# Performance work log

Hardware: AMD Instinct MI355X
Metric: run time of the kernel (lower is better)

## Reference

```python
import jax, jax.numpy as jnp
import numpy as np

EPS_ATTN = 1e-6
EPS_LN = 1e-5


def _layer_norm(x, g, b):
    m = jnp.mean(x, axis=-1, keepdims=True)
    v = jnp.mean((x - m) ** 2, axis=-1, keepdims=True)
    return (x - m) * jax.lax.rsqrt(v + EPS_LN) * g + b


def _linear_attention(q, k, v):
    # q,k,v: [N, L/S, H, D]; elu feature map (+1 keeps values positive)
    q = jax.nn.elu(q) + 1.0
    k = jax.nn.elu(k) + 1.0
    s_len = v.shape[1]
    v = v / s_len
    kv = jnp.einsum('nshd,nshv->nhdv', k, v)            # [N,H,D,D]
    z = 1.0 / (jnp.einsum('nlhd,nhd->nlh', q, k.sum(axis=1)) + EPS_ATTN)
    out = jnp.einsum('nlhd,nhdv->nlhv', q, kv) * z[..., None] * s_len
    return out


def setup_inputs() -> dict:
    key = jax.random.key(0)
    ks = jax.random.split(key, 8)
    N, L, S, H, D = 4, 4096, 4096, 8, 64
    sc = 0.05
    return {
        'x': jax.random.normal(ks[0], (N, L, H, D), jnp.float32),
        'source': jax.random.normal(ks[1], (N, S, H, D), jnp.float32),
        'wq': jax.random.normal(ks[2], (D, D), jnp.float32) * sc,
        'wk': jax.random.normal(ks[3], (D, D), jnp.float32) * sc,
        'wv': jax.random.normal(ks[4], (D, D), jnp.float32) * sc,
        'wmerge': jax.random.normal(ks[5], (D, D), jnp.float32) * sc,
        'w1': jax.random.normal(ks[6], (2 * D, 2 * D), jnp.float32) * sc,
        'w2': jax.random.normal(ks[7], (D, 2 * D), jnp.float32) * sc,
        'g1': jnp.ones((D,), jnp.float32),
        'b1': jnp.zeros((D,), jnp.float32),
        'g2': jnp.ones((D,), jnp.float32),
        'b2': jnp.zeros((D,), jnp.float32),
    }


def reference(x, source, wq, wk, wv, wmerge, w1, w2, g1, b1, g2, b2):
    # projections (torch Linear: y = x @ W.T), applied on last dim D=d_model
    q = jnp.einsum('nlhd,ed->nlhe', x, wq)
    k = jnp.einsum('nshd,ed->nshe', source, wk)
    v = jnp.einsum('nshd,ed->nshe', source, wv)
    message = _linear_attention(q, k, v)                # [N,L,H,D]
    message = jnp.einsum('nlhd,ed->nlhe', message, wmerge)
    message = _layer_norm(message, g1, b1)
    h = jnp.concatenate([x, message], axis=-1)          # [N,L,H,2D]
    h = jax.nn.relu(jnp.einsum('nlhd,ed->nlhe', h, w1))
    h = jnp.einsum('nlhd,ed->nlhe', h, w2)              # [N,L,H,D]
    h = _layer_norm(h, g2, b2)
    return x + h
```

## Files before the change

kernel.cpp:

```cpp
#include <hip/hip_runtime.h>
#include <cstdint>

#define NB 4
#define LL 4096
#define SS 4096
#define HH 8
#define DD 64
#define NHC (NB*HH)
#define KVCH 16

typedef unsigned short ushort_t;
typedef __bf16 bf16x8 __attribute__((ext_vector_type(8)));
typedef float f32x4 __attribute__((ext_vector_type(4)));
typedef unsigned short u16x8 __attribute__((ext_vector_type(8)));
typedef unsigned short u16x4 __attribute__((ext_vector_type(4)));

__device__ __forceinline__ float bf2f(unsigned short u) {
    union { unsigned int i; float f; } v; v.i = ((unsigned int)u) << 16; return v.f;
}
__device__ __forceinline__ unsigned short f2bf(float f) {
    union { __bf16 b; unsigned short u; } v; v.b = (__bf16)f; return v.u;
}
__device__ __forceinline__ bool input_is_bf16(const void* g1) {
    return ((const unsigned short*)g1)[0] == 0x3F80u;
}

template<bool BF16>
__device__ __forceinline__ float ldgf(const void* p, size_t i) {
    if constexpr (BF16) return bf2f(((const unsigned short*)p)[i]);
    else                return ((const float*)p)[i];
}
template<bool BF16>
__device__ __forceinline__ u16x8 ld8(const void* p, size_t i) {
    if constexpr (BF16) {
        return *reinterpret_cast<const u16x8*>((const unsigned short*)p + i);
    } else {
        const f32x4* f4 = reinterpret_cast<const f32x4*>((const float*)p + i);
        f32x4 a = f4[0], b = f4[1];
        u16x8 o;
        #pragma unroll
        for (int j = 0; j < 4; ++j) { o[j] = f2bf(a[j]); o[4 + j] = f2bf(b[j]); }
        return o;
    }
}
__device__ __forceinline__ bf16x8 ldsA(const ushort_t* p) {
    return *reinterpret_cast<const bf16x8*>(p);
}
#define MFMA16(a,b,c) __builtin_amdgcn_mfma_f32_16x16x32_bf16(a,b,c,0,0,0)

template<bool BF16, int LC>
__device__ __forceinline__ void stage_w(const void* g, size_t goff, ushort_t* dst,
                                        int rows, int dstride, int tid) {
    int total8 = (rows << LC) >> 3;
    for (int i8 = tid; i8 < total8; i8 += 256) {
        int i = i8 << 3;
        int r = i >> LC, c = i & ((1 << LC) - 1);
        *reinterpret_cast<u16x8*>(dst + r * dstride + c) = ld8<BF16>(g, goff + i);
    }
}

__device__ __forceinline__ void red16(float v[4]) {
    #pragma unroll
    for (int m = 1; m < 16; m <<= 1) {
        #pragma unroll
        for (int r = 0; r < 4; ++r) v[r] += __shfl_xor(v[r], m);
    }
}

template<bool BF16, bool PART>
__device__ void kv_body(const void* __restrict__ src, const void* __restrict__ wk,
                        const void* __restrict__ wv, float* __restrict__ kvg,
                        float* __restrict__ ksumg,
                        ushort_t* S, ushort_t* KT, ushort_t* VT, float* KS)
{
    const int tid = threadIdx.x;
    const int lane = tid & 63, w = tid >> 6;
    const int lg = lane >> 4, l15 = lane & 15;
    const int bid = blockIdx.x;
    const int nh = bid >> 4, ch = bid & 15;
    const int n = nh >> 3, h = nh & 7;
    const int s0 = ch * 256;
    const f32x4 z4 = {0.f, 0.f, 0.f, 0.f};

    stage_w<BF16, 6>(wk, 0, KT, 64, 136, tid);
    stage_w<BF16, 6>(wv, 0, VT, 64, 136, tid);
    for (int i8 = tid; i8 < 1024; i8 += 256) {
        int r = i8 >> 3, c8 = (i8 & 7) << 3;
        size_t gb = ((size_t)((size_t)n * SS + (s0 + r)) * HH + h) * DD + c8;
        *reinterpret_cast<u16x8*>(S + r * 72 + c8) = ld8<BF16>(src, gb);
    }
    __syncthreads();

    bf16x8 wkf[2][4], wvf[2][4];
    #pragma unroll
    for (int ks = 0; ks < 2; ++ks)
        #pragma unroll
        for (int nt = 0; nt < 4; ++nt) {
            wkf[ks][nt] = ldsA(KT + (nt * 16 + l15) * 136 + ks * 32 + lg * 8);
            wvf[ks][nt] = ldsA(VT + (nt * 16 + l15) * 136 + ks * 32 + lg * 8);
        }
    __syncthreads();

    f32x4 kvacc[4];
    #pragma unroll
    for (int nt = 0; nt < 4; ++nt) kvacc[nt] = z4;
    float ksp[4] = {0.f, 0.f, 0.f, 0.f};

    for (int st = 0; st < 2; ++st) {
        #pragma unroll
        for (int mtt = 0; mtt < 2; ++mtt) {
            const int rowA = w * 32 + mtt * 16;
            bf16x8 af[2];
            #pragma unroll
            for (int ks = 0; ks < 2; ++ks)
                af[ks] = ldsA(S + (rowA + l15) * 72 + ks * 32 + lg * 8);
            f32x4 ka[4], va[4];
            #pragma unroll
            for (int nt = 0; nt < 4; ++nt) { ka[nt] = z4; va[nt] = z4; }
            __builtin_amdgcn_s_setprio(1);
            #pragma unroll
            for (int ks = 0; ks < 2; ++ks)
                #pragma unroll
                for (int nt = 0; nt < 4; ++nt) {
                    ka[nt] = MFMA16(af[ks], wkf[ks][nt], ka[nt]);
                    va[nt] = MFMA16(af[ks], wvf[ks][nt], va[nt]);
                }
            __builtin_amdgcn_s_setprio(0);
            #pragma unroll
            for (int nt = 0; nt < 4; ++nt) {
                u16x4 kp, vp;
                #pragma unroll
                for (int r = 0; r < 4; ++r) {
                    float kvl = ka[nt][r];
                    kvl = kvl > 0.f ? kvl + 1.f : __expf(kvl);
                    ksp[nt] += kvl;
                    kp[r] = f2bf(kvl);
                    vp[r] = f2bf(va[nt][r]);
                }
                const int dcol = nt * 16 + l15;
                *reinterpret_cast<u16x4*>(KT + dcol * 136 + rowA + lg * 4) = kp;
                *reinterpret_cast<u16x4*>(VT + dcol * 136 + rowA + lg * 4) = vp;
            }
        }
        __syncthreads();

        if (st == 0) {
            for (int i8 = tid; i8 < 1024; i8 += 256) {
                int r = i8 >> 3, c8 = (i8 & 7) << 3;
                size_t gb = ((size_t)((size_t)n * SS + (s0 + 128 + r)) * HH + h) * DD + c8;
                *reinterpret_cast<u16x8*>(S + r * 72 + c8) = ld8<BF16>(src, gb);
            }
        }
        __builtin_amdgcn_s_setprio(1);
        #pragma unroll
        for (int ks = 0; ks < 4; ++ks) {
            bf16x8 akv = ldsA(KT + (w * 16 + l15) * 136 + ks * 32 + lg * 8);
            #pragma unroll
            for (int nt = 0; nt < 4; ++nt) {
                bf16x8 bkv = ldsA(VT + (nt * 16 + l15) * 136 + ks * 32 + lg * 8);
                kvacc[nt] = MFMA16(akv, bkv, kvacc[nt]);
            }
        }
        __builtin_amdgcn_s_setprio(0);
        __syncthreads();
    }

    if constexpr (PART) {
        float* kvo = kvg + (size_t)bid * 4096;
        #pragma unroll
        for (int nt = 0; nt < 4; ++nt)
            #pragma unroll
            for (int r = 0; r < 4; ++r)
                kvo[(w * 16 + lg * 4 + r) * DD + nt * 16 + l15] = kvacc[nt][r];
    } else {
        float* kvo = kvg + (size_t)nh * 4096;
        #pragma unroll
        for (int nt = 0; nt < 4; ++nt)
            #pragma unroll
            for (int r = 0; r < 4; ++r)
                atomicAdd(&kvo[(w * 16 + lg * 4 + r) * DD + nt * 16 + l15], kvacc[nt][r]);
    }
    #pragma unroll
    for (int m = 16; m < 64; m <<= 1)
        #pragma unroll
        for (int nt = 0; nt < 4; ++nt) ksp[nt] += __shfl_xor(ksp[nt], m);
    if (lane < 16) {
        #pragma unroll
        for (int nt = 0; nt < 4; ++nt) KS[w * 64 + nt * 16 + lane] = ksp[nt];
    }
    __syncthreads();
    if (tid < 64) {
        float s = KS[tid] + KS[64 + tid] + KS[128 + tid] + KS[192 + tid];
        if constexpr (PART) ksumg[(size_t)bid * 64 + tid] = s;
        else                atomicAdd(&ksumg[nh * 64 + tid], s);
    }
}

template<bool PART>
__global__ __launch_bounds__(256, 2) void kv_kernel(
    const void* __restrict__ src, const void* __restrict__ wk, const void* __restrict__ wv,
    const void* __restrict__ g1, float* __restrict__ kvg, float* __restrict__ ksumg)
{
    __shared__ ushort_t S[128 * 72];
    __shared__ ushort_t KT[64 * 136];
    __shared__ ushort_t VT[64 * 136];
    __shared__ float    KS[4 * 64];
    if (input_is_bf16(g1)) kv_body<true , PART>(src, wk, wv, kvg, ksumg, S, KT, VT, KS);
    else                   kv_body<false, PART>(src, wk, wv, kvg, ksumg, S, KT, VT, KS);
}

template<bool BF16, bool PART>
__device__ void main_body(const void* __restrict__ x,
                          const void* __restrict__ wq, const void* __restrict__ wm,
                          const void* __restrict__ w1, const void* __restrict__ w2,
                          const void* __restrict__ g1, const void* __restrict__ b1,
                          const void* __restrict__ g2, const void* __restrict__ b2,
                          const float* __restrict__ kvg, const float* __restrict__ ksumg,
                          void* __restrict__ outp,
                          ushort_t* w1s, ushort_t* kvs, ushort_t* B0, ushort_t* B1,
                          ushort_t* B2)
{
    const int tid = threadIdx.x;
    const int lane = tid & 63, w = tid >> 6;
    const int lg = lane >> 4, l15 = lane & 15;
    const int bid = blockIdx.x;
    const int nh = bid >> 4, ch = bid & 15;
    const int n = nh >> 3, h = nh & 7;
    const int rowA = w * 16;
    const f32x4 z4 = {0.f, 0.f, 0.f, 0.f};

    auto ldx = [&](int t, u16x8 xv[2]) {
        #pragma unroll
        for (int p = 0; p < 2; ++p) {
            int r16 = p * 8 + (lane >> 3), c8 = (lane & 7) << 3;
            size_t gb = ((size_t)((size_t)n * LL + (ch * 256 + t * 64 + rowA + r16)) * HH + h) * DD + c8;
            xv[p] = ld8<BF16>(x, gb);
        }
    };

    u16x8 xv[2];
    ldx(0, xv);

    stage_w<BF16, 6>(wq, 0, B0, 64, 72, tid);
    stage_w<BF16, 6>(wm, 0, B1, 64, 72, tid);
    stage_w<BF16, 7>(w2, 0, w1s, 64, 136, tid);
    if constexpr (PART) {
        for (int i4 = tid; i4 < 1024; i4 += 256) {
            const float* base = kvg + (size_t)nh * KVCH * 4096 + i4 * 4;
            f32x4 s = z4;
            #pragma unroll
            for (int c = 0; c < KVCH; ++c)
                s += *reinterpret_cast<const f32x4*>(base + c * 4096);
            int d = i4 >> 4, e4 = (i4 * 4) & 63;
            u16x4 pk;
            #pragma unroll
            for (int j = 0; j < 4; ++j) pk[j] = f2bf(s[j]);
            *reinterpret_cast<u16x4*>(B2 + d * 72 + e4) = pk;
        }
    } else {
        for (int i = tid; i < 4096; i += 256) {
            int d = i >> 6, e = i & 63;
            B2[d * 72 + e] = f2bf(kvg[(size_t)nh * 4096 + i]);
        }
    }
    __syncthreads();

    bf16x8 wqf[2][4], w2f[4][4];
    #pragma unroll
    for (int ks = 0; ks < 2; ++ks)
        #pragma unroll
        for (int nt = 0; nt < 4; ++nt)
            wqf[ks][nt] = ldsA(B0 + (nt * 16 + l15) * 72 + ks * 32 + lg * 8);
    #pragma unroll
    for (int ks = 0; ks < 4; ++ks)
        #pragma unroll
        for (int nt = 0; nt < 4; ++nt)
            w2f[ks][nt] = ldsA(w1s + (nt * 16 + l15) * 136 + ks * 32 + lg * 8);
    {
        bf16x8 akv[2];
        #pragma unroll
        for (int ks = 0; ks < 2; ++ks)
            akv[ks] = ldsA(B2 + (w * 16 + l15) * 72 + ks * 32 + lg * 8);
        f32x4 km[4];
        #pragma unroll
        for (int nt = 0; nt < 4; ++nt) km[nt] = z4;
        #pragma unroll
        for (int ks = 0; ks < 2; ++ks)
            #pragma unroll
            for (int nt = 0; nt < 4; ++nt) {
                bf16x8 bwm = ldsA(B1 + (nt * 16 + l15) * 72 + ks * 32 + lg * 8);
                km[nt] = MFMA16(akv[ks], bwm, km[nt]);
            }
        #pragma unroll
        for (int nt = 0; nt < 4; ++nt)
            #pragma unroll
            for (int r = 0; r < 4; ++r)
                kvs[(nt * 16 + l15) * 72 + w * 16 + lg * 4 + r] = f2bf(km[nt][r]);
    }
    __syncthreads();

    stage_w<BF16, 7>(w1, 0, w1s, 128, 136, tid);
    bf16x8 kvmf[2][4];
    #pragma unroll
    for (int ks = 0; ks < 2; ++ks)
        #pragma unroll
        for (int nt = 0; nt < 4; ++nt)
            kvmf[ks][nt] = ldsA(kvs + (nt * 16 + l15) * 72 + ks * 32 + lg * 8);
    float g1r[4], b1r[4], g2r[4], b2r[4], ksr[4];
    #pragma unroll
    for (int nt = 0; nt < 4; ++nt) {
        int c = nt * 16 + l15;
        g1r[nt] = ldgf<BF16>(g1, c); b1r[nt] = ldgf<BF16>(b1, c);
        g2r[nt] = ldgf<BF16>(g2, c); b2r[nt] = ldgf<BF16>(b2, c);
        if constexpr (PART) {
            float s = 0.f;
            #pragma unroll
            for (int cc = 0; cc < KVCH; ++cc)
                s += ksumg[((size_t)nh * KVCH + cc) * 64 + c];
            ksr[nt] = s;
        } else {
            ksr[nt] = ksumg[nh * 64 + c];
        }
    }
    __syncthreads();

    for (int t = 0; t < 4; ++t) {
        const int l0 = ch * 256 + t * 64;

        #pragma unroll
        for (int p = 0; p < 2; ++p) {
            int r16 = p * 8 + (lane >> 3), c8 = (lane & 7) << 3;
            *reinterpret_cast<u16x8*>(B0 + (rowA + r16) * 72 + c8) = xv[p];
        }
        u16x8 xn[2];
        if (t < 3) ldx(t + 1, xn);

        bf16x8 af[2];
        #pragma unroll
        for (int ks = 0; ks < 2; ++ks)
            af[ks] = ldsA(B0 + (rowA + l15) * 72 + ks * 32 + lg * 8);
        f32x4 qa[4];
        #pragma unroll
        for (int nt = 0; nt < 4; ++nt) qa[nt] = z4;
        __builtin_amdgcn_s_setprio(1);
        #pragma unroll
        for (int ks = 0; ks < 2; ++ks)
            #pragma unroll
            for (int nt = 0; nt < 4; ++nt)
                qa[nt] = MFMA16(af[ks], wqf[ks][nt], qa[nt]);
        __builtin_amdgcn_s_setprio(0);
        float zp[4] = {0.f, 0.f, 0.f, 0.f};
        #pragma unroll
        for (int nt = 0; nt < 4; ++nt)
            #pragma unroll
            for (int r = 0; r < 4; ++r) {
                float v = qa[nt][r];
                v = v > 0.f ? v + 1.f : __expf(v);
                zp[r] += v * ksr[nt];
                B1[(rowA + lg * 4 + r) * 72 + nt * 16 + l15] = f2bf(v);
            }
        red16(zp);
        float zr[4];
        #pragma unroll
        for (int r = 0; r < 4; ++r) zr[r] = 1.f / (zp[r] + 1e-6f);

        #pragma unroll
        for (int ks = 0; ks < 2; ++ks)
            af[ks] = ldsA(B1 + (rowA + l15) * 72 + ks * 32 + lg * 8);
        f32x4 ma[4];
        #pragma unroll
        for (int nt = 0; nt < 4; ++nt) ma[nt] = z4;
        __builtin_amdgcn_s_setprio(1);
        #pragma unroll
        for (int ks = 0; ks < 2; ++ks)
            #pragma unroll
            for (int nt = 0; nt < 4; ++nt)
                ma[nt] = MFMA16(af[ks], kvmf[ks][nt], ma[nt]);
        __builtin_amdgcn_s_setprio(0);
        #pragma unroll
        for (int nt = 0; nt < 4; ++nt)
            #pragma unroll
            for (int r = 0; r < 4; ++r) ma[nt][r] *= zr[r];

        float s1[4] = {0.f,0.f,0.f,0.f}, s2[4] = {0.f,0.f,0.f,0.f};
        #pragma unroll
        for (int nt = 0; nt < 4; ++nt)
            #pragma unroll
            for (int r = 0; r < 4; ++r) {
                float v = ma[nt][r]; s1[r] += v; s2[r] += v * v;
            }
        red16(s1); red16(s2);
        #pragma unroll
        for (int r = 0; r < 4; ++r) {
            float mu = s1[r] * 0.015625f;
            float var = s2[r] * 0.015625f - mu * mu;
            s1[r] = mu; s2[r] = rsqrtf(var + 1e-5f);
        }
        #pragma unroll
        for (int nt = 0; nt < 4; ++nt)
            #pragma unroll
            for (int r = 0; r < 4; ++r)
                B1[(rowA + lg * 4 + r) * 72 + nt * 16 + l15] =
                    f2bf((ma[nt][r] - s1[r]) * s2[r] * g1r[nt] + b1r[nt]);

        f32x4 ha[4];
        #pragma unroll
        for (int nt = 0; nt < 4; ++nt) ha[nt] = z4;
        #pragma unroll
        for (int half = 0; half < 2; ++half) {
            f32x4 ta[4];
            #pragma unroll
            for (int nt = 0; nt < 4; ++nt) ta[nt] = z4;
            __builtin_amdgcn_s_setprio(1);
            #pragma unroll
            for (int ks = 0; ks < 4; ++ks) {
                const ushort_t* bp = (ks < 2) ? B0 : B1;
                bf16x8 a1 = ldsA(bp + (rowA + l15) * 72 + (ks & 1) * 32 + lg * 8);
                #pragma unroll
                for (int nt = 0; nt < 4; ++nt) {
                    bf16x8 bw = ldsA(w1s + (half * 64 + nt * 16 + l15) * 136 + ks * 32 + lg * 8);
                    ta[nt] = MFMA16(a1, bw, ta[nt]);
                }
            }
            __builtin_amdgcn_s_setprio(0);
            #pragma unroll
            for (int nt = 0; nt < 4; ++nt)
                #pragma unroll
                for (int r = 0; r < 4; ++r)
                    B2[(rowA + lg * 4 + r) * 72 + nt * 16 + l15] =
                        f2bf(fmaxf(ta[nt][r], 0.f));
            __builtin_amdgcn_s_setprio(1);
            #pragma unroll
            for (int k2 = 0; k2 < 2; ++k2) {
                bf16x8 a2 = ldsA(B2 + (rowA + l15) * 72 + k2 * 32 + lg * 8);
                #pragma unroll
                for (int nt = 0; nt < 4; ++nt)
                    ha[nt] = MFMA16(a2, w2f[half * 2 + k2][nt], ha[nt]);
            }
            __builtin_amdgcn_s_setprio(0);
        }

        float t1[4] = {0.f,0.f,0.f,0.f}, t2[4] = {0.f,0.f,0.f,0.f};
        #pragma unroll
        for (int nt = 0; nt < 4; ++nt)
            #pragma unroll
            for (int r = 0; r < 4; ++r) {
                float v = ha[nt][r]; t1[r] += v; t2[r] += v * v;
            }
        red16(t1); red16(t2);
        #pragma unroll
        for (int r = 0; r < 4; ++r) {
            float mu = t1[r] * 0.015625f;
            float var = t2[r] * 0.015625f - mu * mu;
            t1[r] = mu; t2[r] = rsqrtf(var + 1e-5f);
        }
        #pragma unroll
        for (int nt = 0; nt < 4; ++nt)
            #pragma unroll
            for (int r = 0; r < 4; ++r) {
                float xv2 = bf2f(B0[(rowA + lg * 4 + r) * 72 + nt * 16 + l15]);
                float ov = xv2 + (ha[nt][r] - t1[r]) * t2[r] * g2r[nt] + b2r[nt];
                B1[(rowA + lg * 4 + r) * 72 + nt * 16 + l15] = f2bf(ov);
            }

        #pragma unroll
        for (int p = 0; p < 2; ++p) {
            int r16 = p * 8 + (lane >> 3), c8 = (lane & 7) << 3;
            size_t gb = ((size_t)((size_t)n * LL + (l0 + rowA + r16)) * HH + h) * DD + c8;
            u16x8 v = *reinterpret_cast<const u16x8*>(B1 + (rowA + r16) * 72 + c8);
            if constexpr (BF16) {
                *reinterpret_cast<u16x8*>((unsigned short*)outp + gb) = v;
            } else {
                float* fo = (float*)outp + gb;
                f32x4 lo, hi;
                #pragma unroll
                for (int j = 0; j < 4; ++j) { lo[j] = bf2f(v[j]); hi[j] = bf2f(v[4 + j]); }
                *reinterpret_cast<f32x4*>(fo) = lo;
                *reinterpret_cast<f32x4*>(fo + 4) = hi;
            }
        }

        if (t < 3) { xv[0] = xn[0]; xv[1] = xn[1]; }
    }
}

template<bool PART>
__global__ __launch_bounds__(256, 2) void main_kernel(
    const void* __restrict__ x,
    const void* __restrict__ wq, const void* __restrict__ wm,
    const void* __restrict__ w1, const void* __restrict__ w2,
    const void* __restrict__ g1, const void* __restrict__ b1,
    const void* __restrict__ g2, const void* __restrict__ b2,
    const float* __restrict__ kvg, const float* __restrict__ ksumg,
    void* __restrict__ outp)
{
    __shared__ ushort_t w1s[128 * 136];
    __shared__ ushort_t kvs[64 * 72];
    __shared__ ushort_t B0[64 * 72];
    __shared__ ushort_t B1[64 * 72];
    __shared__ ushort_t B2[64 * 72];
    if (input_is_bf16(g1))
        main_body<true , PART>(x, wq, wm, w1, w2, g1, b1, g2, b2, kvg, ksumg, outp,
                               w1s, kvs, B0, B1, B2);
    else
        main_body<false, PART>(x, wq, wm, w1, w2, g1, b1, g2, b2, kvg, ksumg, outp,
                               w1s, kvs, B0, B1, B2);
}

extern "C" void kernel_launch(void* const* d_in, const int* in_sizes, int n_in,
                              void* d_out, int out_size, void* d_ws, size_t ws_size,
                              hipStream_t stream) {
    const void* x   = d_in[0];
    const void* src = d_in[1];
    const void* wq  = d_in[2];
    const void* wk  = d_in[3];
    const void* wv  = d_in[4];
    const void* wm  = d_in[5];
    const void* w1  = d_in[6];
    const void* w2  = d_in[7];
    const void* g1  = d_in[8];
    const void* b1  = d_in[9];
    const void* g2  = d_in[10];
    const void* b2  = d_in[11];

    const size_t kv_elems   = (size_t)NHC * KVCH * 4096;
    const size_t ksum_elems = (size_t)NHC * KVCH * 64;
    const size_t need = (kv_elems + ksum_elems) * sizeof(float);

    if (ws_size >= need) {
        float* kvp = (float*)d_ws;
        float* ksp = kvp + kv_elems;
        kv_kernel<true ><<<NHC * KVCH, 256, 0, stream>>>(src, wk, wv, g1, kvp, ksp);
        main_kernel<true ><<<NHC * 16, 256, 0, stream>>>(x, wq, wm, w1, w2, g1, b1,
                                                         g2, b2, kvp, ksp, d_out);
    } else {
        float* kvg   = (float*)d_ws;
        float* ksumg = kvg + (size_t)NHC * DD * DD;
        hipMemsetAsync(d_ws, 0, ((size_t)NHC * DD * DD + NHC * DD) * sizeof(float), stream);
        kv_kernel<false><<<NHC * KVCH, 256, 0, stream>>>(src, wk, wv, g1, kvg, ksumg);
        main_kernel<false><<<NHC * 16, 256, 0, stream>>>(x, wq, wm, w1, w2, g1, b1,
                                                         g2, b2, kvg, ksumg, d_out);
    }
}
```

Measured before the change: 160.5 us.

## Split KV reduction into separate kernel, double main grid, swizzle LDS

Adds a reduce kernel that sums the per-chunk KV partials, multiplies by wmerge once per head and writes a bf16 transposed result plus ksum to workspace. Previously every main-kernel block redid this reduction and small GEMM. The main kernel now runs with twice as many blocks, each handling 128 rows, and uses XOR-swizzled unpadded LDS layouts. It also splits the FFN hidden dimension into four 32-wide pieces to shrink the B2 buffer, with launch bounds raised to 3 blocks per CU for higher occupancy. The cost is an extra kernel launch and a workspace round trip for the reduced KV.

```diff
diff --git a/kernel.cpp b/kernel.cpp
--- a/kernel.cpp
+++ b/kernel.cpp
@@ -48,6 +48,9 @@
 }
 #define MFMA16(a,b,c) __builtin_amdgcn_mfma_f32_16x16x32_bf16(a,b,c,0,0,0)
 
+__device__ __forceinline__ int sw64(int r, int c)  { return (r << 6) + (c ^ ((r & 7) << 3)); }
+__device__ __forceinline__ int sw128(int r, int c) { return (r << 7) + (c ^ ((r & 7) << 3)); }
+
 template<bool BF16, int LC>
 __device__ __forceinline__ void stage_w(const void* g, size_t goff, ushort_t* dst,
                                         int rows, int dstride, int tid) {
@@ -56,6 +59,17 @@
         int i = i8 << 3;
         int r = i >> LC, c = i & ((1 << LC) - 1);
         *reinterpret_cast<u16x8*>(dst + r * dstride + c) = ld8<BF16>(g, goff + i);
+    }
+}
+template<bool BF16, int LC>
+__device__ __forceinline__ void stage_sw(const void* g, ushort_t* dst, int rows, int tid) {
+    int total8 = (rows << LC) >> 3;
+    for (int i8 = tid; i8 < total8; i8 += 256) {
+        int i = i8 << 3;
+        int r = i >> LC, c = i & ((1 << LC) - 1);
+        int off;
+        if constexpr (LC == 6) off = sw64(r, c); else off = sw128(r, c);
+        *reinterpret_cast<u16x8*>(dst + off) = ld8<BF16>(g, i);
     }
 }
 
@@ -209,22 +223,91 @@
     else                   kv_body<false, PART>(src, wk, wv, kvg, ksumg, S, KT, VT, KS);
 }
 
-template<bool BF16, bool PART>
+template<bool BF16, int NCH>
+__device__ void reduce_body(const float* __restrict__ kvp, const float* __restrict__ ksp,
+                            const void* __restrict__ wm,
+                            ushort_t* __restrict__ kvmT, float* __restrict__ ksumf,
+                            ushort_t* KVS, ushort_t* WMS)
+{
+    const int tid = threadIdx.x;
+    const int lane = tid & 63, w = tid >> 6;
+    const int lg = lane >> 4, l15 = lane & 15;
+    const int nh = blockIdx.x;
+    const f32x4 z4 = {0.f, 0.f, 0.f, 0.f};
+
+    stage_w<BF16, 6>(wm, 0, WMS, 64, 72, tid);
+    for (int i4 = tid; i4 < 1024; i4 += 256) {
+        const float* base = kvp + (size_t)nh * NCH * 4096 + i4 * 4;
+        f32x4 s = z4;
+        #pragma unroll
+        for (int c = 0; c < NCH; ++c)
+            s += *reinterpret_cast<const f32x4*>(base + c * 4096);
+        int d = i4 >> 4, e4 = (i4 & 15) * 4;
+        u16x4 pk;
+        #pragma unroll
+        for (int j = 0; j < 4; ++j) pk[j] = f2bf(s[j]);
+        *reinterpret_cast<u16x4*>(KVS + d * 72 + e4) = pk;
+    }
+    if (tid < 64) {
+        float s = 0.f;
+        #pragma unroll
+        for (int c = 0; c < NCH; ++c) s += ksp[((size_t)nh * NCH + c) * 64 + tid];
+        ksumf[nh * 64 + tid] = s;
+    }
+    __syncthreads();
+
+    bf16x8 akv[2];
+    #pragma unroll
+    for (int ks = 0; ks < 2; ++ks)
+        akv[ks] = ldsA(KVS + (w * 16 + l15) * 72 + ks * 32 + lg * 8);
+    f32x4 km[4];
+    #pragma unroll
+    for (int nt = 0; nt < 4; ++nt) km[nt] = z4;
+    #pragma unroll
+    for (int ks = 0; ks < 2; ++ks)
+        #pragma unroll
+        for (int nt = 0; nt < 4; ++nt) {
+            bf16x8 bwm = ldsA(WMS + (nt * 16 + l15) * 72 + ks * 32 + lg * 8);
+            km[nt] = MFMA16(akv[ks], bwm, km[nt]);
+        }
+    #pragma unroll
+    for (int nt = 0; nt < 4; ++nt) {
+        u16x4 pk;
+        #pragma unroll
+        for (int r = 0; r < 4; ++r) pk[r] = f2bf(km[nt][r]);
+        *reinterpret_cast<u16x4*>(kvmT + (size_t)nh * 4096 + (nt * 16 + l15) * 64
+                                  + w * 16 + lg * 4) = pk;
+    }
+}
+
+template<int NCH>
+__global__ __launch_bounds__(256, 4) void reduce_kernel(
+    const float* __restrict__ kvp, const float* __restrict__ ksp,
+    const void* __restrict__ wm, const void* __restrict__ g1,
+    ushort_t* __restrict__ kvmT, float* __restrict__ ksumf)
+{
+    __shared__ ushort_t KVS[64 * 72];
+    __shared__ ushort_t WMS[64 * 72];
+    if (input_is_bf16(g1)) reduce_body<true , NCH>(kvp, ksp, wm, kvmT, ksumf, KVS, WMS);
+    else                   reduce_body<false, NCH>(kvp, ksp, wm, kvmT, ksumf, KVS, WMS);
+}
+
+template<bool BF16>
 __device__ void main_body(const void* __restrict__ x,
-                          const void* __restrict__ wq, const void* __restrict__ wm,
+                          const void* __restrict__ wq,
                           const void* __restrict__ w1, const void* __restrict__ w2,
                           const void* __restrict__ g1, const void* __restrict__ b1,
                           const void* __restrict__ g2, const void* __restrict__ b2,
-                          const float* __restrict__ kvg, const float* __restrict__ ksumg,
+                          const ushort_t* __restrict__ kvmT,
+                          const float* __restrict__ ksumf,
                           void* __restrict__ outp,
-                          ushort_t* w1s, ushort_t* kvs, ushort_t* B0, ushort_t* B1,
-                          ushort_t* B2)
+                          ushort_t* w1s, ushort_t* B0, ushort_t* B1, ushort_t* B2)
 {
     const int tid = threadIdx.x;
     const int lane = tid & 63, w = tid >> 6;
     const int lg = lane >> 4, l15 = lane & 15;
     const int bid = blockIdx.x;
-    const int nh = bid >> 4, ch = bid & 15;
+    const int nh = bid >> 5, ch = bid & 31;
     const int n = nh >> 3, h = nh & 7;
     const int rowA = w * 16;
     const f32x4 z4 = {0.f, 0.f, 0.f, 0.f};
@@ -233,7 +316,7 @@
         #pragma unroll
         for (int p = 0; p < 2; ++p) {
             int r16 = p * 8 + (lane >> 3), c8 = (lane & 7) << 3;
-            size_t gb = ((size_t)((size_t)n * LL + (ch * 256 + t * 64 + rowA + r16)) * HH + h) * DD + c8;
+            size_t gb = ((size_t)((size_t)n * LL + (ch * 128 + t * 64 + rowA + r16)) * HH + h) * DD + c8;
             xv[p] = ld8<BF16>(x, gb);
         }
     };
@@ -241,104 +324,55 @@
     u16x8 xv[2];
     ldx(0, xv);
 
-    stage_w<BF16, 6>(wq, 0, B0, 64, 72, tid);
-    stage_w<BF16, 6>(wm, 0, B1, 64, 72, tid);
-    stage_w<BF16, 7>(w2, 0, w1s, 64, 136, tid);
-    if constexpr (PART) {
-        for (int i4 = tid; i4 < 1024; i4 += 256) {
-            const float* base = kvg + (size_t)nh * KVCH * 4096 + i4 * 4;
-            f32x4 s = z4;
-            #pragma unroll
-            for (int c = 0; c < KVCH; ++c)
-                s += *reinterpret_cast<const f32x4*>(base + c * 4096);
-            int d = i4 >> 4, e4 = (i4 * 4) & 63;
-            u16x4 pk;
-            #pragma unroll
-            for (int j = 0; j < 4; ++j) pk[j] = f2bf(s[j]);
-            *reinterpret_cast<u16x4*>(B2 + d * 72 + e4) = pk;
-        }
-    } else {
-        for (int i = tid; i < 4096; i += 256) {
-            int d = i >> 6, e = i & 63;
-            B2[d * 72 + e] = f2bf(kvg[(size_t)nh * 4096 + i]);
-        }
-    }
-    __syncthreads();
-
-    bf16x8 wqf[2][4], w2f[4][4];
+    stage_sw<BF16, 6>(wq, B0, 64, tid);
+    stage_sw<BF16, 7>(w2, w1s, 64, tid);
+    __syncthreads();
+
+    bf16x8 wqf[2][4], w2f[4][4], kvmf[2][4];
     #pragma unroll
     for (int ks = 0; ks < 2; ++ks)
         #pragma unroll
         for (int nt = 0; nt < 4; ++nt)
-            wqf[ks][nt] = ldsA(B0 + (nt * 16 + l15) * 72 + ks * 32 + lg * 8);
-    #pragma unroll
-    for (int ks = 0; ks < 4; ++ks)
-        #pragma unroll
-        for (int nt = 0; nt < 4; ++nt)
-            w2f[ks][nt] = ldsA(w1s + (nt * 16 + l15) * 136 + ks * 32 + lg * 8);
-    {
-        bf16x8 akv[2];
-        #pragma unroll
-        for (int ks = 0; ks < 2; ++ks)
-            akv[ks] = ldsA(B2 + (w * 16 + l15) * 72 + ks * 32 + lg * 8);
-        f32x4 km[4];
-        #pragma unroll
-        for (int nt = 0; nt < 4; ++nt) km[nt] = z4;
-        #pragma unroll
-        for (int ks = 0; ks < 2; ++ks)
-            #pragma unroll
-            for (int nt = 0; nt < 4; ++nt) {
-                bf16x8 bwm = ldsA(B1 + (nt * 16 + l15) * 72 + ks * 32 + lg * 8);
-                km[nt] = MFMA16(akv[ks], bwm, km[nt]);
-            }
-        #pragma unroll
-        for (int nt = 0; nt < 4; ++nt)
-            #pragma unroll
-            for (int r = 0; r < 4; ++r)
-                kvs[(nt * 16 + l15) * 72 + w * 16 + lg * 4 + r] = f2bf(km[nt][r]);
-    }
-    __syncthreads();
-
-    stage_w<BF16, 7>(w1, 0, w1s, 128, 136, tid);
-    bf16x8 kvmf[2][4];
+            wqf[ks][nt] = ldsA(B0 + sw64(nt * 16 + l15, ks * 32 + lg * 8));
+    #pragma unroll
+    for (int q = 0; q < 4; ++q)
+        #pragma unroll
+        for (int nt = 0; nt < 4; ++nt)
+            w2f[q][nt] = ldsA(w1s + sw128(nt * 16 + l15, q * 32 + lg * 8));
     #pragma unroll
     for (int ks = 0; ks < 2; ++ks)
         #pragma unroll
         for (int nt = 0; nt < 4; ++nt)
-            kvmf[ks][nt] = ldsA(kvs + (nt * 16 + l15) * 72 + ks * 32 + lg * 8);
+            kvmf[ks][nt] = *reinterpret_cast<const bf16x8*>(
+                kvmT + (size_t)nh * 4096 + (nt * 16 + l15) * 64 + ks * 32 + lg * 8);
     float g1r[4], b1r[4], g2r[4], b2r[4], ksr[4];
     #pragma unroll
     for (int nt = 0; nt < 4; ++nt) {
         int c = nt * 16 + l15;
         g1r[nt] = ldgf<BF16>(g1, c); b1r[nt] = ldgf<BF16>(b1, c);
         g2r[nt] = ldgf<BF16>(g2, c); b2r[nt] = ldgf<BF16>(b2, c);
-        if constexpr (PART) {
-            float s = 0.f;
-            #pragma unroll
-            for (int cc = 0; cc < KVCH; ++cc)
-                s += ksumg[((size_t)nh * KVCH + cc) * 64 + c];
-            ksr[nt] = s;
-        } else {
-            ksr[nt] = ksumg[nh * 64 + c];
-        }
-    }
-    __syncthreads();
-
-    for (int t = 0; t < 4; ++t) {
-        const int l0 = ch * 256 + t * 64;
+        ksr[nt] = ksumf[nh * 64 + c];
+    }
+    __syncthreads();
+
+    stage_sw<BF16, 7>(w1, w1s, 128, tid);
+    __syncthreads();
+
+    for (int t = 0; t < 2; ++t) {
+        const int l0 = ch * 128 + t * 64;
 
         #pragma unroll
         for (int p = 0; p < 2; ++p) {
             int r16 = p * 8 + (lane >> 3), c8 = (lane & 7) << 3;
-            *reinterpret_cast<u16x8*>(B0 + (rowA + r16) * 72 + c8) = xv[p];
+            *reinterpret_cast<u16x8*>(B0 + sw64(rowA + r16, c8)) = xv[p];
         }
         u16x8 xn[2];
-        if (t < 3) ldx(t + 1, xn);
+        if (t == 0) ldx(1, xn);
 
         bf16x8 af[2];
         #pragma unroll
         for (int ks = 0; ks < 2; ++ks)
-            af[ks] = ldsA(B0 + (rowA + l15) * 72 + ks * 32 + lg * 8);
+            af[ks] = ldsA(B0 + sw64(rowA + l15, ks * 32 + lg * 8));
         f32x4 qa[4];
         #pragma unroll
         for (int nt = 0; nt < 4; ++nt) qa[nt] = z4;
@@ -357,7 +391,7 @@
                 float v = qa[nt][r];
                 v = v > 0.f ? v + 1.f : __expf(v);
                 zp[r] += v * ksr[nt];
-                B1[(rowA + lg * 4 + r) * 72 + nt * 16 + l15] = f2bf(v);
+                B1[sw64(rowA + lg * 4 + r, nt * 16 + l15)] = f2bf(v);
             }
         red16(zp);
         float zr[4];
@@ -366,7 +400,7 @@
 
         #pragma unroll
         for (int ks = 0; ks < 2; ++ks)
-            af[ks] = ldsA(B1 + (rowA + l15) * 72 + ks * 32 + lg * 8);
+            af[ks] = ldsA(B1 + sw64(rowA + l15, ks * 32 + lg * 8));
         f32x4 ma[4];
         #pragma unroll
         for (int nt = 0; nt < 4; ++nt) ma[nt] = z4;
@@ -400,43 +434,39 @@
         for (int nt = 0; nt < 4; ++nt)
             #pragma unroll
             for (int r = 0; r < 4; ++r)
-                B1[(rowA + lg * 4 + r) * 72 + nt * 16 + l15] =
+                B1[sw64(rowA + lg * 4 + r, nt * 16 + l15)] =
                     f2bf((ma[nt][r] - s1[r]) * s2[r] * g1r[nt] + b1r[nt]);
 
         f32x4 ha[4];
         #pragma unroll
         for (int nt = 0; nt < 4; ++nt) ha[nt] = z4;
         #pragma unroll
-        for (int half = 0; half < 2; ++half) {
-            f32x4 ta[4];
-            #pragma unroll
-            for (int nt = 0; nt < 4; ++nt) ta[nt] = z4;
+        for (int q = 0; q < 4; ++q) {
+            f32x4 ta[2];
+            ta[0] = z4; ta[1] = z4;
             __builtin_amdgcn_s_setprio(1);
             #pragma unroll
             for (int ks = 0; ks < 4; ++ks) {
                 const ushort_t* bp = (ks < 2) ? B0 : B1;
-                bf16x8 a1 = ldsA(bp + (rowA + l15) * 72 + (ks & 1) * 32 + lg * 8);
+                bf16x8 a1 = ldsA(bp + sw64(rowA + l15, (ks & 1) * 32 + lg * 8));
                 #pragma unroll
-                for (int nt = 0; nt < 4; ++nt) {
-                    bf16x8 bw = ldsA(w1s + (half * 64 + nt * 16 + l15) * 136 + ks * 32 + lg * 8);
+                for (int nt = 0; nt < 2; ++nt) {
+                    bf16x8 bw = ldsA(w1s + sw128(q * 32 + nt * 16 + l15, ks * 32 + lg * 8));
                     ta[nt] = MFMA16(a1, bw, ta[nt]);
                 }
             }
             __builtin_amdgcn_s_setprio(0);
             #pragma unroll
-            for (int nt = 0; nt < 4; ++nt)
+            for (int nt = 0; nt < 2; ++nt)
                 #pragma unroll
                 for (int r = 0; r < 4; ++r)
-                    B2[(rowA + lg * 4 + r) * 72 + nt * 16 + l15] =
+                    B2[(rowA + lg * 4 + r) * 40 + nt * 16 + l15] =
                         f2bf(fmaxf(ta[nt][r], 0.f));
+            bf16x8 a2 = ldsA(B2 + (rowA + l15) * 40 + lg * 8);
             __builtin_amdgcn_s_setprio(1);
             #pragma unroll
-            for (int k2 = 0; k2 < 2; ++k2) {
-                bf16x8 a2 = ldsA(B2 + (rowA + l15) * 72 + k2 * 32 + lg * 8);
-                #pragma unroll
-                for (int nt = 0; nt < 4; ++nt)
-                    ha[nt] = MFMA16(a2, w2f[half * 2 + k2][nt], ha[nt]);
-            }
+            for (int nt = 0; nt < 4; ++nt)
+                ha[nt] = MFMA16(a2, w2f[q][nt], ha[nt]);
             __builtin_amdgcn_s_setprio(0);
         }
 
@@ -458,16 +488,16 @@
         for (int nt = 0; nt < 4; ++nt)
             #pragma unroll
             for (int r = 0; r < 4; ++r) {
-                float xv2 = bf2f(B0[(rowA + lg * 4 + r) * 72 + nt * 16 + l15]);
+                float xv2 = bf2f(B0[sw64(rowA + lg * 4 + r, nt * 16 + l15)]);
                 float ov = xv2 + (ha[nt][r] - t1[r]) * t2[r] * g2r[nt] + b2r[nt];
-                B1[(rowA + lg * 4 + r) * 72 + nt * 16 + l15] = f2bf(ov);
+                B1[sw64(rowA + lg * 4 + r, nt * 16 + l15)] = f2bf(ov);
             }
 
         #pragma unroll
         for (int p = 0; p < 2; ++p) {
             int r16 = p * 8 + (lane >> 3), c8 = (lane & 7) << 3;
             size_t gb = ((size_t)((size_t)n * LL + (l0 + rowA + r16)) * HH + h) * DD + c8;
-            u16x8 v = *reinterpret_cast<const u16x8*>(B1 + (rowA + r16) * 72 + c8);
+            u16x8 v = *reinterpret_cast<const u16x8*>(B1 + sw64(rowA + r16, c8));
             if constexpr (BF16) {
                 *reinterpret_cast<u16x8*>((unsigned short*)outp + gb) = v;
             } else {
@@ -480,31 +510,29 @@
             }
         }
 
-        if (t < 3) { xv[0] = xn[0]; xv[1] = xn[1]; }
-    }
-}
-
-template<bool PART>
-__global__ __launch_bounds__(256, 2) void main_kernel(
+        if (t == 0) { xv[0] = xn[0]; xv[1] = xn[1]; }
+    }
+}
+
+__global__ __launch_bounds__(256, 3) void main_kernel(
     const void* __restrict__ x,
-    const void* __restrict__ wq, const void* __restrict__ wm,
+    const void* __restrict__ wq,
     const void* __restrict__ w1, const void* __restrict__ w2,
     const void* __restrict__ g1, const void* __restrict__ b1,
     const void* __restrict__ g2, const void* __restrict__ b2,
-    const float* __restrict__ kvg, const float* __restrict__ ksumg,
+    const ushort_t* __restrict__ kvmT, const float* __restrict__ ksumf,
     void* __restrict__ outp)
 {
-    __shared__ ushort_t w1s[128 * 136];
-    __shared__ ushort_t kvs[64 * 72];
-    __shared__ ushort_t B0[64 * 72];
-    __shared__ ushort_t B1[64 * 72];
-    __shared__ ushort_t B2[64 * 72];
+    __shared__ ushort_t w1s[128 * 128];
+    __shared__ ushort_t B0[64 * 64];
+    __shared__ ushort_t B1[64 * 64];
+    __shared__ ushort_t B2[64 * 40];
     if (input_is_bf16(g1))
-        main_body<true , PART>(x, wq, wm, w1, w2, g1, b1, g2, b2, kvg, ksumg, outp,
-                               w1s, kvs, B0, B1, B2);
+        main_body<true >(x, wq, w1, w2, g1, b1, g2, b2, kvmT, ksumf, outp,
+                         w1s, B0, B1, B2);
     else
-        main_body<false, PART>(x, wq, wm, w1, w2, g1, b1, g2, b2, kvg, ksumg, outp,
-                               w1s, kvs, B0, B1, B2);
+        main_body<false>(x, wq, w1, w2, g1, b1, g2, b2, kvmT, ksumf, outp,
+                         w1s, B0, B1, B2);
 }
 
 extern "C" void kernel_launch(void* const* d_in, const int* in_sizes, int n_in,
@@ -523,22 +551,31 @@
     const void* g2  = d_in[10];
     const void* b2  = d_in[11];
 
-    const size_t kv_elems   = (size_t)NHC * KVCH * 4096;
-    const size_t ksum_elems = (size_t)NHC * KVCH * 64;
-    const size_t need = (kv_elems + ksum_elems) * sizeof(float);
-
-    if (ws_size >= need) {
-        float* kvp = (float*)d_ws;
-        float* ksp = kvp + kv_elems;
+    const size_t kv16   = (size_t)NHC * KVCH * 4096;
+    const size_t ks16   = (size_t)NHC * KVCH * 64;
+    const size_t need16 = (kv16 + ks16) * sizeof(float) + (size_t)NHC * 4096 * 2
+                        + (size_t)NHC * 64 * sizeof(float);
+
+    if (ws_size >= need16) {
+        float*    kvp   = (float*)d_ws;
+        float*    ksp   = kvp + kv16;
+        ushort_t* kvmT  = (ushort_t*)(ksp + ks16);
+        float*    ksumf = (float*)(kvmT + (size_t)NHC * 4096);
         kv_kernel<true ><<<NHC * KVCH, 256, 0, stream>>>(src, wk, wv, g1, kvp, ksp);
-        main_kernel<true ><<<NHC * 16, 256, 0, stream>>>(x, wq, wm, w1, w2, g1, b1,
-                                                         g2, b2, kvp, ksp, d_out);
+        reduce_kernel<KVCH><<<NHC, 256, 0, stream>>>(kvp, ksp, wm, g1, kvmT, ksumf);
+        main_kernel<<<NHC * 32, 256, 0, stream>>>(x, wq, w1, w2, g1, b1, g2, b2,
+                                                  kvmT, ksumf, d_out);
     } else {
-        float* kvg   = (float*)d_ws;
-        float* ksumg = kvg + (size_t)NHC * DD * DD;
-        hipMemsetAsync(d_ws, 0, ((size_t)NHC * DD * DD + NHC * DD) * sizeof(float), stream);
-        kv_kernel<false><<<NHC * KVCH, 256, 0, stream>>>(src, wk, wv, g1, kvg, ksumg);
-        main_kernel<false><<<NHC * 16, 256, 0, stream>>>(x, wq, wm, w1, w2, g1, b1,
-                                                         g2, b2, kvg, ksumg, d_out);
-    }
-}
+        const size_t kv1 = (size_t)NHC * 4096;
+        const size_t ks1 = (size_t)NHC * 64;
+        float*    kvp   = (float*)d_ws;
+        float*    ksp   = kvp + kv1;
+        ushort_t* kvmT  = (ushort_t*)(ksp + ks1);
+        float*    ksumf = (float*)(kvmT + (size_t)NHC * 4096);
+        hipMemsetAsync(d_ws, 0, (kv1 + ks1) * sizeof(float), stream);
+        kv_kernel<false><<<NHC * KVCH, 256, 0, stream>>>(src, wk, wv, g1, kvp, ksp);
+        reduce_kernel<1><<<NHC, 256, 0, stream>>>(kvp, ksp, wm, g1, kvmT, ksumf);
+        main_kernel<<<NHC * 32, 256, 0, stream>>>(x, wq, w1, w2, g1, b1, g2, b2,
+                                                  kvmT, ksumf, d_out);
+    }
+}
```

Measured after the change: 226.0 us. 1.41x slower.

## Move partial KV reduction and merge projection into a separate small kernel

Applied to the files above, without the earlier changes.

Adds a reduce kernel that sums the per-chunk KV and k-sum partials once per head and multiplies by the merge weight, storing a bf16 transposed result. Before this, each of the 16 main-kernel blocks per head redid that reduction and the small matmul. The main kernel now loads the precomputed matrix straight from global memory, which removes one LDS staging buffer and a sync. The cost is an extra kernel launch, and the tiny 128-block reduce kernel sits on the critical path between the other two.

```diff
diff --git a/kernel.cpp b/kernel.cpp
--- a/kernel.cpp
+++ b/kernel.cpp
@@ -209,16 +209,86 @@
     else                   kv_body<false, PART>(src, wk, wv, kvg, ksumg, S, KT, VT, KS);
 }
 
-template<bool BF16, bool PART>
+template<bool BF16, int NCH>
+__device__ void reduce_body(const float* __restrict__ kvp, const float* __restrict__ ksp,
+                            const void* __restrict__ wm,
+                            ushort_t* __restrict__ kvmT, float* __restrict__ ksumf)
+{
+    const int lane = threadIdx.x & 63;
+    const int lg = lane >> 4, l15 = lane & 15;
+    const int bid = blockIdx.x;
+    const int nh = bid >> 2, q4 = bid & 3;
+    const int d0 = q4 * 16;
+    const f32x4 z4 = {0.f, 0.f, 0.f, 0.f};
+
+    f32x4 sa[2][2];
+    #pragma unroll
+    for (int ks = 0; ks < 2; ++ks) { sa[ks][0] = z4; sa[ks][1] = z4; }
+    #pragma unroll
+    for (int c = 0; c < NCH; ++c) {
+        const float* base = kvp + ((size_t)nh * NCH + c) * 4096 + (d0 + l15) * 64;
+        #pragma unroll
+        for (int ks = 0; ks < 2; ++ks) {
+            const f32x4* p4 = reinterpret_cast<const f32x4*>(base + ks * 32 + lg * 8);
+            sa[ks][0] += p4[0];
+            sa[ks][1] += p4[1];
+        }
+    }
+    bf16x8 af[2];
+    #pragma unroll
+    for (int ks = 0; ks < 2; ++ks)
+        #pragma unroll
+        for (int j = 0; j < 8; ++j)
+            af[ks][j] = (__bf16)((j < 4) ? sa[ks][0][j] : sa[ks][1][j - 4]);
+
+    f32x4 km[4];
+    #pragma unroll
+    for (int nt = 0; nt < 4; ++nt) km[nt] = z4;
+    #pragma unroll
+    for (int ks = 0; ks < 2; ++ks)
+        #pragma unroll
+        for (int nt = 0; nt < 4; ++nt) {
+            u16x8 t = ld8<BF16>(wm, (size_t)(nt * 16 + l15) * 64 + ks * 32 + lg * 8);
+            bf16x8 bwm = *reinterpret_cast<bf16x8*>(&t);
+            km[nt] = MFMA16(af[ks], bwm, km[nt]);
+        }
+    #pragma unroll
+    for (int nt = 0; nt < 4; ++nt) {
+        u16x4 pk;
+        #pragma unroll
+        for (int r = 0; r < 4; ++r) pk[r] = f2bf(km[nt][r]);
+        *reinterpret_cast<u16x4*>(kvmT + (size_t)nh * 4096 + (nt * 16 + l15) * 64
+                                  + d0 + lg * 4) = pk;
+    }
+
+    if (q4 == 0) {
+        float s = 0.f;
+        #pragma unroll
+        for (int c = 0; c < NCH; ++c) s += ksp[((size_t)nh * NCH + c) * 64 + lane];
+        ksumf[nh * 64 + lane] = s;
+    }
+}
+
+template<int NCH>
+__global__ __launch_bounds__(64) void reduce_kernel(
+    const float* __restrict__ kvp, const float* __restrict__ ksp,
+    const void* __restrict__ wm, const void* __restrict__ g1,
+    ushort_t* __restrict__ kvmT, float* __restrict__ ksumf)
+{
+    if (input_is_bf16(g1)) reduce_body<true , NCH>(kvp, ksp, wm, kvmT, ksumf);
+    else                   reduce_body<false, NCH>(kvp, ksp, wm, kvmT, ksumf);
+}
+
+template<bool BF16>
 __device__ void main_body(const void* __restrict__ x,
-                          const void* __restrict__ wq, const void* __restrict__ wm,
+                          const void* __restrict__ wq,
                           const void* __restrict__ w1, const void* __restrict__ w2,
                           const void* __restrict__ g1, const void* __restrict__ b1,
                           const void* __restrict__ g2, const void* __restrict__ b2,
-                          const float* __restrict__ kvg, const float* __restrict__ ksumg,
+                          const ushort_t* __restrict__ kvmT,
+                          const float* __restrict__ ksumf,
                           void* __restrict__ outp,
-                          ushort_t* w1s, ushort_t* kvs, ushort_t* B0, ushort_t* B1,
-                          ushort_t* B2)
+                          ushort_t* w1s, ushort_t* B0, ushort_t* B1, ushort_t* B2)
 {
     const int tid = threadIdx.x;
     const int lane = tid & 63, w = tid >> 6;
@@ -242,86 +312,34 @@
     ldx(0, xv);
 
     stage_w<BF16, 6>(wq, 0, B0, 64, 72, tid);
-    stage_w<BF16, 6>(wm, 0, B1, 64, 72, tid);
     stage_w<BF16, 7>(w2, 0, w1s, 64, 136, tid);
-    if constexpr (PART) {
-        for (int i4 = tid; i4 < 1024; i4 += 256) {
-            const float* base = kvg + (size_t)nh * KVCH * 4096 + i4 * 4;
-            f32x4 s = z4;
-            #pragma unroll
-            for (int c = 0; c < KVCH; ++c)
-                s += *reinterpret_cast<const f32x4*>(base + c * 4096);
-            int d = i4 >> 4, e4 = (i4 * 4) & 63;
-            u16x4 pk;
-            #pragma unroll
-            for (int j = 0; j < 4; ++j) pk[j] = f2bf(s[j]);
-            *reinterpret_cast<u16x4*>(B2 + d * 72 + e4) = pk;
-        }
-    } else {
-        for (int i = tid; i < 4096; i += 256) {
-            int d = i >> 6, e = i & 63;
-            B2[d * 72 + e] = f2bf(kvg[(size_t)nh * 4096 + i]);
-        }
-    }
     __syncthreads();
 
-    bf16x8 wqf[2][4], w2f[4][4];
+    bf16x8 wqf[2][4], w2f[4][4], kvmf[2][4];
     #pragma unroll
     for (int ks = 0; ks < 2; ++ks)
         #pragma unroll
-        for (int nt = 0; nt < 4; ++nt)
+        for (int nt = 0; nt < 4; ++nt) {
             wqf[ks][nt] = ldsA(B0 + (nt * 16 + l15) * 72 + ks * 32 + lg * 8);
+            kvmf[ks][nt] = *reinterpret_cast<const bf16x8*>(
+                kvmT + (size_t)nh * 4096 + (nt * 16 + l15) * 64 + ks * 32 + lg * 8);
+        }
     #pragma unroll
     for (int ks = 0; ks < 4; ++ks)
         #pragma unroll
         for (int nt = 0; nt < 4; ++nt)
             w2f[ks][nt] = ldsA(w1s + (nt * 16 + l15) * 136 + ks * 32 + lg * 8);
-    {
-        bf16x8 akv[2];
-        #pragma unroll
-        for (int ks = 0; ks < 2; ++ks)
-            akv[ks] = ldsA(B2 + (w * 16 + l15) * 72 + ks * 32 + lg * 8);
-        f32x4 km[4];
-        #pragma unroll
-        for (int nt = 0; nt < 4; ++nt) km[nt] = z4;
-        #pragma unroll
-        for (int ks = 0; ks < 2; ++ks)
-            #pragma unroll
-            for (int nt = 0; nt < 4; ++nt) {
-                bf16x8 bwm = ldsA(B1 + (nt * 16 + l15) * 72 + ks * 32 + lg * 8);
-                km[nt] = MFMA16(akv[ks], bwm, km[nt]);
-            }
-        #pragma unroll
-        for (int nt = 0; nt < 4; ++nt)
-            #pragma unroll
-            for (int r = 0; r < 4; ++r)
-                kvs[(nt * 16 + l15) * 72 + w * 16 + lg * 4 + r] = f2bf(km[nt][r]);
-    }
-    __syncthreads();
-
-    stage_w<BF16, 7>(w1, 0, w1s, 128, 136, tid);
-    bf16x8 kvmf[2][4];
-    #pragma unroll
-    for (int ks = 0; ks < 2; ++ks)
-        #pragma unroll
-        for (int nt = 0; nt < 4; ++nt)
-            kvmf[ks][nt] = ldsA(kvs + (nt * 16 + l15) * 72 + ks * 32 + lg * 8);
     float g1r[4], b1r[4], g2r[4], b2r[4], ksr[4];
     #pragma unroll
     for (int nt = 0; nt < 4; ++nt) {
         int c = nt * 16 + l15;
         g1r[nt] = ldgf<BF16>(g1, c); b1r[nt] = ldgf<BF16>(b1, c);
         g2r[nt] = ldgf<BF16>(g2, c); b2r[nt] = ldgf<BF16>(b2, c);
-        if constexpr (PART) {
-            float s = 0.f;
-            #pragma unroll
-            for (int cc = 0; cc < KVCH; ++cc)
-                s += ksumg[((size_t)nh * KVCH + cc) * 64 + c];
-            ksr[nt] = s;
-        } else {
-            ksr[nt] = ksumg[nh * 64 + c];
-        }
-    }
+        ksr[nt] = ksumf[nh * 64 + c];
+    }
+    __syncthreads();
+
+    stage_w<BF16, 7>(w1, 0, w1s, 128, 136, tid);
     __syncthreads();
 
     for (int t = 0; t < 4; ++t) {
@@ -484,27 +502,25 @@
     }
 }
 
-template<bool PART>
 __global__ __launch_bounds__(256, 2) void main_kernel(
     const void* __restrict__ x,
-    const void* __restrict__ wq, const void* __restrict__ wm,
+    const void* __restrict__ wq,
     const void* __restrict__ w1, const void* __restrict__ w2,
     const void* __restrict__ g1, const void* __restrict__ b1,
     const void* __restrict__ g2, const void* __restrict__ b2,
-    const float* __restrict__ kvg, const float* __restrict__ ksumg,
+    const ushort_t* __restrict__ kvmT, const float* __restrict__ ksumf,
     void* __restrict__ outp)
 {
     __shared__ ushort_t w1s[128 * 136];
-    __shared__ ushort_t kvs[64 * 72];
     __shared__ ushort_t B0[64 * 72];
     __shared__ ushort_t B1[64 * 72];
     __shared__ ushort_t B2[64 * 72];
     if (input_is_bf16(g1))
-        main_body<true , PART>(x, wq, wm, w1, w2, g1, b1, g2, b2, kvg, ksumg, outp,
-                               w1s, kvs, B0, B1, B2);
+        main_body<true >(x, wq, w1, w2, g1, b1, g2, b2, kvmT, ksumf, outp,
+                         w1s, B0, B1, B2);
     else
-        main_body<false, PART>(x, wq, wm, w1, w2, g1, b1, g2, b2, kvg, ksumg, outp,
-                               w1s, kvs, B0, B1, B2);
+        main_body<false>(x, wq, w1, w2, g1, b1, g2, b2, kvmT, ksumf, outp,
+                         w1s, B0, B1, B2);
 }
 
 extern "C" void kernel_launch(void* const* d_in, const int* in_sizes, int n_in,
@@ -523,22 +539,31 @@
     const void* g2  = d_in[10];
     const void* b2  = d_in[11];
 
-    const size_t kv_elems   = (size_t)NHC * KVCH * 4096;
-    const size_t ksum_elems = (size_t)NHC * KVCH * 64;
-    const size_t need = (kv_elems + ksum_elems) * sizeof(float);
-
-    if (ws_size >= need) {
-        float* kvp = (float*)d_ws;
-        float* ksp = kvp + kv_elems;
+    const size_t kv16   = (size_t)NHC * KVCH * 4096;
+    const size_t ks16   = (size_t)NHC * KVCH * 64;
+    const size_t need16 = (kv16 + ks16) * sizeof(float) + (size_t)NHC * 4096 * 2
+                        + (size_t)NHC * 64 * sizeof(float);
+
+    if (ws_size >= need16) {
+        float*    kvp   = (float*)d_ws;
+        float*    ksp   = kvp + kv16;
+        ushort_t* kvmT  = (ushort_t*)(ksp + ks16);
+        float*    ksumf = (float*)(kvmT + (size_t)NHC * 4096);
         kv_kernel<true ><<<NHC * KVCH, 256, 0, stream>>>(src, wk, wv, g1, kvp, ksp);
-        main_kernel<true ><<<NHC * 16, 256, 0, stream>>>(x, wq, wm, w1, w2, g1, b1,
-                                                         g2, b2, kvp, ksp, d_out);
+        reduce_kernel<KVCH><<<NHC * 4, 64, 0, stream>>>(kvp, ksp, wm, g1, kvmT, ksumf);
+        main_kernel<<<NHC * 16, 256, 0, stream>>>(x, wq, w1, w2, g1, b1, g2, b2,
+                                                  kvmT, ksumf, d_out);
     } else {
-        float* kvg   = (float*)d_ws;
-        float* ksumg = kvg + (size_t)NHC * DD * DD;
-        hipMemsetAsync(d_ws, 0, ((size_t)NHC * DD * DD + NHC * DD) * sizeof(float), stream);
-        kv_kernel<false><<<NHC * KVCH, 256, 0, stream>>>(src, wk, wv, g1, kvg, ksumg);
-        main_kernel<false><<<NHC * 16, 256, 0, stream>>>(x, wq, wm, w1, w2, g1, b1,
-                                                         g2, b2, kvg, ksumg, d_out);
-    }
-}
+        const size_t kv1 = (size_t)NHC * 4096;
+        const size_t ks1 = (size_t)NHC * 64;
+        float*    kvp   = (float*)d_ws;
+        float*    ksp   = kvp + kv1;
+        ushort_t* kvmT  = (ushort_t*)(ksp + ks1);
+        float*    ksumf = (float*)(kvmT + (size_t)NHC * 4096);
+        hipMemsetAsync(d_ws, 0, (kv1 + ks1) * sizeof(float), stream);
+        kv_kernel<false><<<NHC * KVCH, 256, 0, stream>>>(src, wk, wv, g1, kvp, ksp);
+        reduce_kernel<1><<<NHC * 4, 64, 0, stream>>>(kvp, ksp, wm, g1, kvmT, ksumf);
+        main_kernel<<<NHC * 16, 256, 0, stream>>>(x, wq, w1, w2, g1, b1, g2, b2,
+                                                  kvmT, ksumf, d_out);
+    }
+}
```

New measurement: 160.1 us. No clear change (-0.2%).
